# Performance work log

Measured on AMD Instinct MI355X. Metric: run time of the kernel, lower is better.

Reference implementation:

```python
import jax, jax.numpy as jnp
import numpy as np

H_, W_, KNN, KO = 64, 64, 32, 32
TAU, ETA, LAMBDA0, ALPHA = 1.5, 8.0, 0.001, 10.0
A_, B_, BETA, BETA_P = 1.0, 0.0, 8.0, 8.0
SMOOTH_KS, SMOOTH_SIGMA, EPS = 5, 1.0, 1e-6


def _base_grid(h, w):
    ys = jnp.arange(h, dtype=jnp.float32)
    xs = jnp.arange(w, dtype=jnp.float32)
    yy, xx = jnp.meshgrid(ys, xs, indexing='ij')
    return jnp.stack([xx.reshape(-1), yy.reshape(-1)], axis=-1)  # (N,2) as (x,y)


def _offset_bins(K_o, h, w):
    maxr = (h ** 2 + w ** 2) ** 0.5 * 0.5
    ks = jnp.arange(1, K_o + 1, dtype=jnp.float32)
    angles = 2.0 * jnp.pi * (ks - 1) / K_o
    radii = 0.2 * maxr + 0.6 * maxr * (ks - 1) / (K_o - 1 + 1e-9)
    return jnp.stack([radii * jnp.cos(angles), radii * jnp.sin(angles)], axis=-1)  # (K_o,2)


def _gaussian_kernel(ks, sigma):
    ax = jnp.arange(-(ks // 2), ks // 2 + 1, dtype=jnp.float32)  # matches torch -ks//2+1 .. ks//2 for odd ks
    xx, yy = jnp.meshgrid(ax, ax, indexing='ij')
    k = jnp.exp(-(xx ** 2 + yy ** 2) / (2.0 * sigma ** 2))
    return (k / k.sum()).reshape(1, 1, ks, ks)


def setup_inputs() -> dict:
    key = jax.random.key(0)
    k1, k2 = jax.random.split(key)
    B, N = 2, H_ * W_
    E = jax.random.normal(k1, (B, N, 256), dtype=jnp.float32)
    A0 = jax.random.uniform(k2, (B, N, N), dtype=jnp.float32)
    return {
        'E': E,
        'A0': A0,
        'P': _base_grid(H_, W_),
        'bins': _offset_bins(KO, H_, W_),
        'smooth_kernel': _gaussian_kernel(SMOOTH_KS, SMOOTH_SIGMA),
    }


def reference(E, A0, P, bins, smooth_kernel):
    B, N, _ = A0.shape
    # top-k neighbors per row (sorted descending, like torch.topk)
    topk_vals, topk_idx = jax.lax.top_k(A0, KNN)  # (B,N,k)

    # offset vectors to neighbors
    p_j = P[topk_idx]                              # (B,N,k,2)
    v = p_j - P[None, :, None, :]                  # (B,N,k,2)
    diff = v[..., None, :] - bins[None, None, None, :, :]   # (B,N,k,K_o,2)
    dist2 = (diff ** 2).sum(-1)                    # (B,N,k,K_o)
    kappa = jnp.exp(-dist2 / (2.0 * TAU ** 2 + 1e-12))

    # global bin histogram and softmax weights
    Hbins = (topk_vals[..., None] * kappa).sum(axis=(1, 2))   # (B,K_o)
    Wsoft = jax.nn.softmax(ETA * Hbins, axis=-1)              # (B,K_o)

    R_edges = LAMBDA0 + (Wsoft[:, None, None, :] * kappa).sum(-1)  # (B,N,k)
    tildeA = topk_vals * R_edges
    A1_edges = tildeA / (tildeA.sum(-1, keepdims=True) + EPS)

    # entropy -> backgroundness U
    p = jax.nn.softmax(ALPHA * A1_edges, axis=-1)
    entropy = -(p * jnp.log(p + EPS)).sum(-1)      # (B,N)
    U = jax.nn.sigmoid(-A_ * entropy + B_)
    m = 1.0 - U

    # mask both endpoints of each edge
    m_j = jax.vmap(jnp.take)(m, topk_idx)          # (B,N,k)
    hatA = m[:, :, None] * A1_edges * m_j
    A2_edges = hatA / (hatA.sum(-1, keepdims=True) + EPS)

    # scatter sparse edges back to dense NxN (row indices unique per row)
    b_idx = jnp.arange(B)[:, None, None]
    n_idx = jnp.arange(N)[None, :, None]
    A2_dense = jnp.zeros((B, N, N), A2_edges.dtype).at[b_idx, n_idx, topk_idx].set(A2_edges)
    A2_dense = A2_dense / (A2_dense.sum(-1, keepdims=True) + EPS)

    # directional evidence
    exp_fwd = jnp.exp(BETA * A2_dense)
    exp_rev = jnp.swapaxes(exp_fwd, -1, -2)
    P_dir = exp_fwd / (exp_fwd + exp_rev + EPS)
    eye = jnp.eye(N, dtype=A2_dense.dtype)
    P_dir = P_dir * (1.0 - eye)                    # zero diagonal
    s_ev = (A2_dense * P_dir).sum(-1)
    A2_T = jnp.swapaxes(A2_dense, -1, -2)
    t_ev = (A2_T * (1.0 - jnp.swapaxes(P_dir, -1, -2))).sum(-1)
    pi_src = s_ev / (s_ev + t_ev + EPS)
    pi_tgt = 1.0 - pi_src

    # spatial attention map
    W_mean = Wsoft.mean(0)                         # (K_o,)
    chi = (kappa * W_mean[None, None, None, :]).sum(-1)       # (B,N,k)
    w_local = jax.nn.softmax(BETA_P * A2_edges, axis=-1)
    q = (w_local * chi).sum(-1)                    # (B,N)
    A1_map = q.reshape(B, 1, H_, W_)
    pad = SMOOTH_KS // 2
    smoothed = jax.lax.conv_general_dilated(A1_map, smooth_kernel, (1, 1), [(pad, pad), (pad, pad)])
    A1_map = jax.nn.sigmoid(smoothed)              # (B,1,h,w)

    return (A2_dense, U, pi_src, pi_tgt, A1_map)
```

## Files before the change

### kernel.cpp

```cpp
#include <hip/hip_runtime.h>
#include <math.h>

#define NN 4096
#define KK 32
#define KOb 32
#define BB 2

constexpr float EPS = 1e-6f;

#define WS_VALS   0
#define WS_IDX    (WS_VALS + BB*NN*KK)
#define WS_HB     (WS_IDX + BB*NN*KK)
#define WS_WSOFT  (WS_HB + BB*KOb)
#define WS_WMEAN  (WS_WSOFT + BB*KOb)
#define WS_A1     (WS_WMEAN + KOb)
#define WS_M      (WS_A1 + BB*NN*KK)
#define WS_CHI    (WS_M + BB*NN)
#define WS_A2     (WS_CHI + BB*NN*KK)
#define WS_SEV    (WS_A2 + BB*NN*KK)
#define WS_TEV    (WS_SEV + BB*NN)
#define WS_Q      (WS_TEV + BB*NN)

#define OUT_A2   0
#define OUT_U    ((size_t)BB*NN*NN)
#define OUT_PSRC (OUT_U + BB*NN)
#define OUT_PTGT (OUT_PSRC + BB*NN)
#define OUT_MAP  (OUT_PTGT + BB*NN)

__device__ __forceinline__ unsigned int fkey(float x) {
    unsigned int u = __float_as_uint(x);
    return u ^ ((unsigned int)((int)u >> 31) | 0x80000000u);
}
__device__ __forceinline__ float key2f(unsigned int k) {
    unsigned int u = (k & 0x80000000u) ? (k ^ 0x80000000u) : ~k;
    return __uint_as_float(u);
}

__global__ __launch_bounds__(256) void k_topk(const float* __restrict__ A0,
                                              float* __restrict__ ws) {
    __shared__ unsigned long long cand[4][128];

    const int t = threadIdx.x;
    const int wv = t >> 6, lane = t & 63;
    const int R = blockIdx.x * 4 + wv;

    if (blockIdx.x == 0 && t < BB * KOb) ws[WS_HB + t] = 0.f;

    const float4* row4 = (const float4*)(A0 + (size_t)R * NN);
    unsigned int key[64];
    #pragma unroll
    for (int j4 = 0; j4 < 16; ++j4) {
        const float4 f = row4[j4 * 64 + lane];
        key[4 * j4 + 0] = fkey(f.x);
        key[4 * j4 + 1] = fkey(f.y);
        key[4 * j4 + 2] = fkey(f.z);
        key[4 * j4 + 3] = fkey(f.w);
    }

    unsigned int lo = 0u, hi = 0xFFFFFFFFu;
    int cnt = NN;
    int it = 0;
    while (cnt > 128) {
        unsigned int mid;
        if (it == 0)      mid = 0xBF7E0000u;
        else if (it == 1) mid = 0xBF7C4000u;
        else              mid = lo + ((hi - lo) >> 1);
        if (mid <= lo || mid >= hi) mid = lo + ((hi - lo) >> 1);
        if (mid == lo) break;
        int c = 0;
        #pragma unroll
        for (int j = 0; j < 64; ++j) c += (key[j] > mid) ? 1 : 0;
        #pragma unroll
        for (int m = 32; m >= 1; m >>= 1) c += __shfl_xor(c, m);
        if (c >= KK) { lo = mid; cnt = c; } else hi = mid;
        if (++it > 48) break;
    }

    int base = 0;
    #pragma unroll
    for (int j = 0; j < 64; ++j) {
        const bool p = key[j] > lo;
        const unsigned long long m = __ballot(p);
        if (p) {
            const int slot = base + __popcll(m & ((1ull << lane) - 1ull));
            if (slot < 128) {
                const unsigned int gidx = (unsigned int)((j >> 2) * 256 + lane * 4 + (j & 3));
                cand[wv][slot] = ((unsigned long long)key[j] << 32)
                               | (unsigned long long)(4095u - gidx);
            }
        }
        base += __popcll(m);
    }
    const int ncand = (base < 128) ? base : 128;
    __syncthreads();

    unsigned long long c0 = (lane < ncand) ? cand[wv][lane] : 0ull;
    unsigned long long c1 = (lane + 64 < ncand) ? cand[wv][lane + 64] : 0ull;
    unsigned long long resk = 0ull;
    for (int r = 0; r < KK; ++r) {
        unsigned long long bst = (c0 > c1) ? c0 : c1;
        #pragma unroll
        for (int m = 32; m >= 1; m >>= 1) {
            const unsigned long long o = __shfl_xor(bst, m);
            if (o > bst) bst = o;
        }
        if (lane == r) resk = bst;
        if (c0 == bst) c0 = 0ull;
        if (c1 == bst) c1 = 0ull;
    }
    if (lane < KK) {
        const unsigned int k = (unsigned int)(resk >> 32);
        const int gidx = 4095 - (int)(resk & 0xFFFull);
        ws[WS_VALS + (size_t)R * KK + lane] = key2f(k);
        ((int*)(ws + WS_IDX))[(size_t)R * KK + lane] = gidx;
    }
}

__global__ __launch_bounds__(256) void k_hbins(const float* __restrict__ bins,
                                               float* __restrict__ ws) {
    __shared__ float lval[1024], ldx[1024], ldy[1024];
    __shared__ float part[8][KOb];
    const int blk = blockIdx.x;
    const int t = threadIdx.x;
    const int row0 = blk * 32;
    const int b = row0 / NN;

    for (int e = t; e < 1024; e += 256) {
        const int R = row0 + (e >> 5);
        const int k = e & 31;
        const int r = R - b * NN;
        const int c = ((int*)(ws + WS_IDX))[(size_t)R * KK + k];
        lval[e] = ws[WS_VALS + (size_t)R * KK + k];
        ldx[e] = (float)((c & 63) - (r & 63));
        ldy[e] = (float)((c >> 6) - (r >> 6));
    }
    __syncthreads();

    const int o = t & 31, g = t >> 5;
    const float bx = bins[2 * o], by = bins[2 * o + 1];
    float acc = 0.f;
    for (int e = g; e < 1024; e += 8) {
        const float dx = ldx[e] - bx, dy = ldy[e] - by;
        acc += lval[e] * __expf(-(dx * dx + dy * dy) * (1.0f / 4.5f));
    }
    part[g][o] = acc;
    __syncthreads();
    if (t < 32) {
        float s = 0.f;
        #pragma unroll
        for (int g2 = 0; g2 < 8; ++g2) s += part[g2][t];
        atomicAdd(ws + WS_HB + b * KOb + t, s);
    }
}

__global__ void k_wsoft(float* __restrict__ ws) {
    __shared__ float sw[64];
    const int t = threadIdx.x;
    const int b = t >> 5, o = t & 31;
    const float h = 8.0f * ws[WS_HB + b * KOb + o];
    float mx = h;
    #pragma unroll
    for (int m = 16; m >= 1; m >>= 1) mx = fmaxf(mx, __shfl_xor(mx, m));
    const float e = __expf(h - mx);
    float s = e;
    #pragma unroll
    for (int m = 16; m >= 1; m >>= 1) s += __shfl_xor(s, m);
    const float w = e / s;
    ws[WS_WSOFT + b * KOb + o] = w;
    sw[t] = w;
    __syncthreads();
    if (t < 32) ws[WS_WMEAN + t] = 0.5f * (sw[t] + sw[32 + t]);
}

__global__ __launch_bounds__(256) void k_row1(const float* __restrict__ bins,
                                              float* __restrict__ ws,
                                              float* __restrict__ out_u) {
    __shared__ float sbins[2 * KOb], swsoft[BB * KOb], swmean[KOb];
    const int t = threadIdx.x;
    if (t < 2 * KOb) sbins[t] = bins[t];
    if (t >= 64 && t < 64 + BB * KOb) swsoft[t - 64] = ws[WS_WSOFT + t - 64];
    if (t >= 128 && t < 128 + KOb) swmean[t - 128] = ws[WS_WMEAN + t - 128];
    __syncthreads();

    const int wv = t >> 6, lane = t & 63;
    const int R = blockIdx.x * 4 + wv;
    const int b = R >> 12;
    const int r = R & (NN - 1);
    const bool act = lane < 32;
    const int k = lane;

    float val = 0.f, Redge = 0.f, chi = 0.f;
    if (act) {
        val = ws[WS_VALS + (size_t)R * KK + k];
        const int c = ((int*)(ws + WS_IDX))[(size_t)R * KK + k];
        const float dx0 = (float)((c & 63) - (r & 63));
        const float dy0 = (float)((c >> 6) - (r >> 6));
        float racc = 0.f, cacc = 0.f;
        for (int o = 0; o < KOb; ++o) {
            const float dx = dx0 - sbins[2 * o], dy = dy0 - sbins[2 * o + 1];
            const float kap = __expf(-(dx * dx + dy * dy) * (1.0f / 4.5f));
            racc += swsoft[b * KOb + o] * kap;
            cacc += swmean[o] * kap;
        }
        Redge = 0.001f + racc;
        chi = cacc;
    }
    const float tilde = act ? val * Redge : 0.f;
    float s = tilde;
    #pragma unroll
    for (int m = 16; m >= 1; m >>= 1) s += __shfl_xor(s, m);
    const float a1 = tilde / (s + EPS);

    const float z = act ? 10.f * a1 : -1e30f;
    float mz = z;
    #pragma unroll
    for (int m = 16; m >= 1; m >>= 1) mz = fmaxf(mz, __shfl_xor(mz, m));
    const float e = act ? __expf(z - mz) : 0.f;
    float se = e;
    #pragma unroll
    for (int m = 16; m >= 1; m >>= 1) se += __shfl_xor(se, m);
    const float p = e / se;
    const float ent_t = act ? -p * __logf(p + EPS) : 0.f;
    float ent = ent_t;
    #pragma unroll
    for (int m = 16; m >= 1; m >>= 1) ent += __shfl_xor(ent, m);
    const float U = 1.f / (1.f + __expf(ent));

    if (act) {
        ws[WS_A1  + (size_t)R * KK + k] = a1;
        ws[WS_CHI + (size_t)R * KK + k] = chi;
    }
    if (lane == 0) { out_u[R] = U; ws[WS_M + R] = 1.f - U; }
}

__global__ __launch_bounds__(256) void k_row2(float* __restrict__ ws) {
    const int gid = blockIdx.x * 256 + threadIdx.x;
    if (gid < BB * NN) ws[WS_TEV + gid] = 0.f;

    const int t = threadIdx.x;
    const int wv = t >> 6, lane = t & 63;
    const int R = blockIdx.x * 4 + wv;
    const int b = R >> 12;
    const bool act = lane < 32;
    const int k = lane;

    const float mi = ws[WS_M + R];
    float a1 = 0.f; int c = 0; float mj = 0.f;
    if (act) {
        a1 = ws[WS_A1 + (size_t)R * KK + k];
        c = ((int*)(ws + WS_IDX))[(size_t)R * KK + k];
        mj = ws[WS_M + b * NN + c];
    }
    const float hat = act ? mi * a1 * mj : 0.f;
    float S = hat;
    #pragma unroll
    for (int m = 16; m >= 1; m >>= 1) S += __shfl_xor(S, m);
    const float a2e = hat / (S + EPS);
    float S2 = a2e;
    #pragma unroll
    for (int m = 16; m >= 1; m >>= 1) S2 += __shfl_xor(S2, m);
    const float dv = a2e / (S2 + EPS);
    if (act) ws[WS_A2 + (size_t)R * KK + k] = dv;

    const float z = act ? 8.f * a2e : -1e30f;
    float mz = z;
    #pragma unroll
    for (int m = 16; m >= 1; m >>= 1) mz = fmaxf(mz, __shfl_xor(mz, m));
    const float e = act ? __expf(z - mz) : 0.f;
    float se = e;
    #pragma unroll
    for (int m = 16; m >= 1; m >>= 1) se += __shfl_xor(se, m);
    const float wl = e / se;
    const float chi = act ? ws[WS_CHI + (size_t)R * KK + k] : 0.f;
    float q = act ? wl * chi : 0.f;
    #pragma unroll
    for (int m = 16; m >= 1; m >>= 1) q += __shfl_xor(q, m);
    if (lane == 0) ws[WS_Q + R] = q;
}

__global__ __launch_bounds__(256) void k_dense(const float* __restrict__ ws,
                                               float* __restrict__ outA2) {
    __shared__ float srow[NN];
    __shared__ int   sidx[KK];
    __shared__ float sval[KK];
    const int R = blockIdx.x;
    const int b = R >> 12;
    const int r = R & (NN - 1);
    const int t = threadIdx.x;

    if (t < KK) {
        sidx[t] = ((const int*)(ws + WS_IDX))[(size_t)R * KK + t];
        sval[t] = ws[WS_A2 + (size_t)R * KK + t];
    }
    float4* s4 = (float4*)srow;
    const float4 z4 = make_float4(0.f, 0.f, 0.f, 0.f);
    #pragma unroll
    for (int i = 0; i < 4; ++i) s4[t + 256 * i] = z4;
    __syncthreads();
    if (t < KK) srow[sidx[t]] = sval[t];
    __syncthreads();
    float4* o4 = (float4*)(outA2 + (size_t)b * NN * NN + (size_t)r * NN);
    #pragma unroll
    for (int i = 0; i < 4; ++i) o4[t + 256 * i] = s4[t + 256 * i];
}

__global__ __launch_bounds__(256) void k_dir(float* __restrict__ ws,
                                             const float* __restrict__ A2d) {
    const int t = threadIdx.x;
    const int wv = t >> 6, lane = t & 63;
    const int R = blockIdx.x * 4 + wv;
    const int b = R >> 12;
    const int r = R & (NN - 1);
    const bool act = lane < 32;
    const int k = lane;

    float a = 0.f; int c = r;
    if (act) {
        a = ws[WS_A2 + (size_t)R * KK + k];
        c = ((int*)(ws + WS_IDX))[(size_t)R * KK + k];
    }
    float pdir = 0.f;
    if (act && c != r) {
        const float arev = A2d[(size_t)b * NN * NN + (size_t)c * NN + r];
        const float ef = __expf(8.f * a), er = __expf(8.f * arev);
        pdir = ef / (ef + er + EPS);
    }
    float s = a * pdir;
    #pragma unroll
    for (int m = 16; m >= 1; m >>= 1) s += __shfl_xor(s, m);
    if (lane == 0) ws[WS_SEV + R] = s;
    if (act) atomicAdd(ws + WS_TEV + b * NN + c, a * (1.f - pdir));
}

__global__ void k_tail(const float* __restrict__ ws, const float* __restrict__ kern,
                       float* __restrict__ out_psrc, float* __restrict__ out_ptgt,
                       float* __restrict__ out_map) {
    const int i = blockIdx.x * 256 + threadIdx.x;
    const float s = ws[WS_SEV + i], tv = ws[WS_TEV + i];
    const float ps = s / (s + tv + EPS);
    out_psrc[i] = ps;
    out_ptgt[i] = 1.f - ps;

    const int b = i >> 12;
    const int pix = i & 4095;
    const int y = pix >> 6, x = pix & 63;
    float acc = 0.f;
    #pragma unroll
    for (int ky = 0; ky < 5; ++ky) {
        const int yy = y + ky - 2;
        if (yy < 0 || yy >= 64) continue;
        #pragma unroll
        for (int kx = 0; kx < 5; ++kx) {
            const int xx = x + kx - 2;
            if (xx < 0 || xx >= 64) continue;
            acc += ws[WS_Q + b * 4096 + yy * 64 + xx] * kern[ky * 5 + kx];
        }
    }
    out_map[i] = 1.f / (1.f + __expf(-acc));
}

extern "C" void kernel_launch(void* const* d_in, const int* in_sizes, int n_in,
                              void* d_out, int out_size, void* d_ws, size_t ws_size,
                              hipStream_t stream) {
    const float* A0   = (const float*)d_in[1];
    const float* bins = (const float*)d_in[3];
    const float* kern = (const float*)d_in[4];
    float* out = (float*)d_out;
    float* ws  = (float*)d_ws;

    k_topk <<<BB * NN / 4,   256, 0, stream>>>(A0, ws);
    k_hbins<<<256,           256, 0, stream>>>(bins, ws);
    k_wsoft<<<1,              64, 0, stream>>>(ws);
    k_row1 <<<BB * NN / 4,   256, 0, stream>>>(bins, ws, out + OUT_U);
    k_row2 <<<BB * NN / 4,   256, 0, stream>>>(ws);
    k_dense<<<BB * NN,       256, 0, stream>>>(ws, out);
    k_dir  <<<BB * NN / 4,   256, 0, stream>>>(ws, out);
    k_tail <<<BB * NN / 256, 256, 0, stream>>>(ws, kern,
                                               out + OUT_PSRC, out + OUT_PTGT,
                                               out + OUT_MAP);
}
```

Measured before the change: 341.6 us.

## Fuse histogram into top-k, fold softmax into row1, merge row2 with dense scatter

Computes the per-bin histogram contribution inside the top-k kernel using shared-memory atomics and a slotted partial buffer, then reduces the partials and applies the softmax in each k_row1 block. This removes the k_hbins and k_wsoft launches. k_row2 is merged into the dense-row writer. The candidate pool shrinks to 64 and is compacted with a prefix scan and ranked by pairwise comparison instead of an iterative max extraction. The catch is that every row1 block redundantly re-reduces the partials, and the histogram now relies on atomics.

New measurement: 333.9 us. 2.2% less time.

```diff
diff --git a/kernel.cpp b/kernel.cpp
--- a/kernel.cpp
+++ b/kernel.cpp
@@ -5,15 +5,14 @@
 #define KK 32
 #define KOb 32
 #define BB 2
+#define NSLOT 64
 
 constexpr float EPS = 1e-6f;
 
 #define WS_VALS   0
 #define WS_IDX    (WS_VALS + BB*NN*KK)
-#define WS_HB     (WS_IDX + BB*NN*KK)
-#define WS_WSOFT  (WS_HB + BB*KOb)
-#define WS_WMEAN  (WS_WSOFT + BB*KOb)
-#define WS_A1     (WS_WMEAN + KOb)
+#define WS_HBP    (WS_IDX + BB*NN*KK)
+#define WS_A1     (WS_HBP + BB*NSLOT*KOb)
 #define WS_M      (WS_A1 + BB*NN*KK)
 #define WS_CHI    (WS_M + BB*NN)
 #define WS_A2     (WS_CHI + BB*NN*KK)
@@ -37,14 +36,20 @@
 }
 
 __global__ __launch_bounds__(256) void k_topk(const float* __restrict__ A0,
+                                              const float* __restrict__ bins,
                                               float* __restrict__ ws) {
-    __shared__ unsigned long long cand[4][128];
+    __shared__ unsigned long long cand[4][64];
+    __shared__ float sbins[2 * KOb];
+    __shared__ float shb[KOb];
 
     const int t = threadIdx.x;
     const int wv = t >> 6, lane = t & 63;
     const int R = blockIdx.x * 4 + wv;
-
-    if (blockIdx.x == 0 && t < BB * KOb) ws[WS_HB + t] = 0.f;
+    const int b = blockIdx.x >> 10;
+    const int r = R & (NN - 1);
+
+    if (t < 2 * KOb) sbins[t] = bins[t];
+    if (t < KOb) shb[t] = 0.f;
 
     const float4* row4 = (const float4*)(A0 + (size_t)R * NN);
     unsigned int key[64];
@@ -58,128 +63,117 @@
     }
 
     unsigned int lo = 0u, hi = 0xFFFFFFFFu;
-    int cnt = NN;
-    int it = 0;
-    while (cnt > 128) {
+    int cnt = NN, myc = 64, it = 0;
+    while (cnt > 64) {
         unsigned int mid;
         if (it == 0)      mid = 0xBF7E0000u;
         else if (it == 1) mid = 0xBF7C4000u;
         else              mid = lo + ((hi - lo) >> 1);
         if (mid <= lo || mid >= hi) mid = lo + ((hi - lo) >> 1);
         if (mid == lo) break;
-        int c = 0;
-        #pragma unroll
-        for (int j = 0; j < 64; ++j) c += (key[j] > mid) ? 1 : 0;
+        int cl = 0;
+        #pragma unroll
+        for (int j = 0; j < 64; ++j) cl += (key[j] > mid) ? 1 : 0;
+        int c = cl;
         #pragma unroll
         for (int m = 32; m >= 1; m >>= 1) c += __shfl_xor(c, m);
-        if (c >= KK) { lo = mid; cnt = c; } else hi = mid;
+        if (c >= KK) { lo = mid; cnt = c; myc = cl; } else hi = mid;
         if (++it > 48) break;
     }
-
-    int base = 0;
+    if (lo == 0u) {
+        int cl = 0;
+        #pragma unroll
+        for (int j = 0; j < 64; ++j) cl += (key[j] > 0u) ? 1 : 0;
+        myc = cl;
+    }
+
+    int pre = myc;
+    #pragma unroll
+    for (int m = 1; m < 64; m <<= 1) {
+        const int o = __shfl_up(pre, m);
+        if (lane >= m) pre += o;
+    }
+    pre -= myc;
+
+    int slot = pre;
     #pragma unroll
     for (int j = 0; j < 64; ++j) {
-        const bool p = key[j] > lo;
-        const unsigned long long m = __ballot(p);
-        if (p) {
-            const int slot = base + __popcll(m & ((1ull << lane) - 1ull));
-            if (slot < 128) {
-                const unsigned int gidx = (unsigned int)((j >> 2) * 256 + lane * 4 + (j & 3));
-                cand[wv][slot] = ((unsigned long long)key[j] << 32)
-                               | (unsigned long long)(4095u - gidx);
-            }
-        }
-        base += __popcll(m);
-    }
-    const int ncand = (base < 128) ? base : 128;
-    __syncthreads();
-
-    unsigned long long c0 = (lane < ncand) ? cand[wv][lane] : 0ull;
-    unsigned long long c1 = (lane + 64 < ncand) ? cand[wv][lane + 64] : 0ull;
-    unsigned long long resk = 0ull;
-    for (int r = 0; r < KK; ++r) {
-        unsigned long long bst = (c0 > c1) ? c0 : c1;
-        #pragma unroll
-        for (int m = 32; m >= 1; m >>= 1) {
-            const unsigned long long o = __shfl_xor(bst, m);
-            if (o > bst) bst = o;
-        }
-        if (lane == r) resk = bst;
-        if (c0 == bst) c0 = 0ull;
-        if (c1 == bst) c1 = 0ull;
-    }
-    if (lane < KK) {
-        const unsigned int k = (unsigned int)(resk >> 32);
-        const int gidx = 4095 - (int)(resk & 0xFFFull);
-        ws[WS_VALS + (size_t)R * KK + lane] = key2f(k);
-        ((int*)(ws + WS_IDX))[(size_t)R * KK + lane] = gidx;
-    }
-}
-
-__global__ __launch_bounds__(256) void k_hbins(const float* __restrict__ bins,
-                                               float* __restrict__ ws) {
-    __shared__ float lval[1024], ldx[1024], ldy[1024];
-    __shared__ float part[8][KOb];
-    const int blk = blockIdx.x;
-    const int t = threadIdx.x;
-    const int row0 = blk * 32;
-    const int b = row0 / NN;
-
-    for (int e = t; e < 1024; e += 256) {
-        const int R = row0 + (e >> 5);
-        const int k = e & 31;
-        const int r = R - b * NN;
-        const int c = ((int*)(ws + WS_IDX))[(size_t)R * KK + k];
-        lval[e] = ws[WS_VALS + (size_t)R * KK + k];
-        ldx[e] = (float)((c & 63) - (r & 63));
-        ldy[e] = (float)((c >> 6) - (r >> 6));
-    }
-    __syncthreads();
-
-    const int o = t & 31, g = t >> 5;
-    const float bx = bins[2 * o], by = bins[2 * o + 1];
-    float acc = 0.f;
-    for (int e = g; e < 1024; e += 8) {
-        const float dx = ldx[e] - bx, dy = ldy[e] - by;
-        acc += lval[e] * __expf(-(dx * dx + dy * dy) * (1.0f / 4.5f));
-    }
-    part[g][o] = acc;
-    __syncthreads();
-    if (t < 32) {
-        float s = 0.f;
-        #pragma unroll
-        for (int g2 = 0; g2 < 8; ++g2) s += part[g2][t];
-        atomicAdd(ws + WS_HB + b * KOb + t, s);
-    }
-}
-
-__global__ void k_wsoft(float* __restrict__ ws) {
-    __shared__ float sw[64];
-    const int t = threadIdx.x;
-    const int b = t >> 5, o = t & 31;
-    const float h = 8.0f * ws[WS_HB + b * KOb + o];
-    float mx = h;
-    #pragma unroll
-    for (int m = 16; m >= 1; m >>= 1) mx = fmaxf(mx, __shfl_xor(mx, m));
-    const float e = __expf(h - mx);
-    float s = e;
-    #pragma unroll
-    for (int m = 16; m >= 1; m >>= 1) s += __shfl_xor(s, m);
-    const float w = e / s;
-    ws[WS_WSOFT + b * KOb + o] = w;
-    sw[t] = w;
-    __syncthreads();
-    if (t < 32) ws[WS_WMEAN + t] = 0.5f * (sw[t] + sw[32 + t]);
+        if (key[j] > lo && slot < 64) {
+            const unsigned int gidx = (unsigned int)((j >> 2) * 256 + lane * 4 + (j & 3));
+            cand[wv][slot] = ((unsigned long long)key[j] << 32)
+                           | (unsigned long long)(4095u - gidx);
+            ++slot;
+        }
+    }
+    const int ncand = (cnt < 64) ? cnt : 64;
+    __syncthreads();
+
+    const unsigned long long cd = (lane < ncand) ? cand[wv][lane] : 0ull;
+    int rank = 0;
+    #pragma unroll
+    for (int i = 0; i < 64; ++i) {
+        const unsigned long long o = __shfl(cd, i);
+        rank += (o > cd) ? 1 : 0;
+    }
+
+    const bool sel = (lane < ncand) && (rank < KK);
+    float val = 0.f; int gidx = 0;
+    if (sel) {
+        val = key2f((unsigned int)(cd >> 32));
+        gidx = 4095 - (int)(cd & 0xFFFull);
+        ws[WS_VALS + (size_t)R * KK + rank] = val;
+        ((int*)(ws + WS_IDX))[(size_t)R * KK + rank] = gidx;
+    }
+
+    if (sel) {
+        const float dx0 = (float)((gidx & 63) - (r & 63));
+        const float dy0 = (float)((gidx >> 6) - (r >> 6));
+        #pragma unroll
+        for (int oo = 0; oo < KOb; ++oo) {
+            const int o = (oo + lane) & 31;
+            const float dx = dx0 - sbins[2 * o], dy = dy0 - sbins[2 * o + 1];
+            atomicAdd(&shb[o], val * __expf(-(dx * dx + dy * dy) * (1.0f / 4.5f)));
+        }
+    }
+    __syncthreads();
+    if (t < KOb)
+        atomicAdd(ws + WS_HBP + b * (NSLOT * KOb) + (blockIdx.x & (NSLOT - 1)) * KOb + t,
+                  shb[t]);
 }
 
 __global__ __launch_bounds__(256) void k_row1(const float* __restrict__ bins,
                                               float* __restrict__ ws,
                                               float* __restrict__ out_u) {
-    __shared__ float sbins[2 * KOb], swsoft[BB * KOb], swmean[KOb];
+    __shared__ float sbins[2 * KOb], sHB[BB * KOb], swsoft[BB * KOb], swmean[KOb];
     const int t = threadIdx.x;
     if (t < 2 * KOb) sbins[t] = bins[t];
-    if (t >= 64 && t < 64 + BB * KOb) swsoft[t - 64] = ws[WS_WSOFT + t - 64];
-    if (t >= 128 && t < 128 + KOb) swmean[t - 128] = ws[WS_WMEAN + t - 128];
+    if (t >= 64 && t < 64 + BB * KOb) sHB[t - 64] = 0.f;
+    __syncthreads();
+
+    #pragma unroll
+    for (int rep = 0; rep < 2; ++rep) {
+        const int task = t + 256 * rep;
+        const int bo = task & 63;
+        const int sg = task >> 6;
+        float ps = 0.f;
+        #pragma unroll
+        for (int s = 0; s < 8; ++s)
+            ps += ws[WS_HBP + (bo >> 5) * (NSLOT * KOb) + (sg * 8 + s) * KOb + (bo & 31)];
+        atomicAdd(&sHB[bo], ps);
+    }
+    __syncthreads();
+    if (t < BB * KOb) {
+        const float h = 8.0f * sHB[t];
+        float mx = h;
+        #pragma unroll
+        for (int m = 16; m >= 1; m >>= 1) mx = fmaxf(mx, __shfl_xor(mx, m));
+        const float e = __expf(h - mx);
+        float s = e;
+        #pragma unroll
+        for (int m = 16; m >= 1; m >>= 1) s += __shfl_xor(s, m);
+        swsoft[t] = e / s;
+    }
+    if (t < KOb) swmean[t] = 0.5f * (swsoft[t] + swsoft[KOb + t]);
     __syncthreads();
 
     const int wv = t >> 6, lane = t & 63;
@@ -233,71 +227,68 @@
     if (lane == 0) { out_u[R] = U; ws[WS_M + R] = 1.f - U; }
 }
 
-__global__ __launch_bounds__(256) void k_row2(float* __restrict__ ws) {
-    const int gid = blockIdx.x * 256 + threadIdx.x;
-    if (gid < BB * NN) ws[WS_TEV + gid] = 0.f;
-
-    const int t = threadIdx.x;
-    const int wv = t >> 6, lane = t & 63;
-    const int R = blockIdx.x * 4 + wv;
-    const int b = R >> 12;
-    const bool act = lane < 32;
-    const int k = lane;
-
-    const float mi = ws[WS_M + R];
-    float a1 = 0.f; int c = 0; float mj = 0.f;
-    if (act) {
-        a1 = ws[WS_A1 + (size_t)R * KK + k];
-        c = ((int*)(ws + WS_IDX))[(size_t)R * KK + k];
-        mj = ws[WS_M + b * NN + c];
-    }
-    const float hat = act ? mi * a1 * mj : 0.f;
-    float S = hat;
-    #pragma unroll
-    for (int m = 16; m >= 1; m >>= 1) S += __shfl_xor(S, m);
-    const float a2e = hat / (S + EPS);
-    float S2 = a2e;
-    #pragma unroll
-    for (int m = 16; m >= 1; m >>= 1) S2 += __shfl_xor(S2, m);
-    const float dv = a2e / (S2 + EPS);
-    if (act) ws[WS_A2 + (size_t)R * KK + k] = dv;
-
-    const float z = act ? 8.f * a2e : -1e30f;
-    float mz = z;
-    #pragma unroll
-    for (int m = 16; m >= 1; m >>= 1) mz = fmaxf(mz, __shfl_xor(mz, m));
-    const float e = act ? __expf(z - mz) : 0.f;
-    float se = e;
-    #pragma unroll
-    for (int m = 16; m >= 1; m >>= 1) se += __shfl_xor(se, m);
-    const float wl = e / se;
-    const float chi = act ? ws[WS_CHI + (size_t)R * KK + k] : 0.f;
-    float q = act ? wl * chi : 0.f;
-    #pragma unroll
-    for (int m = 16; m >= 1; m >>= 1) q += __shfl_xor(q, m);
-    if (lane == 0) ws[WS_Q + R] = q;
-}
-
-__global__ __launch_bounds__(256) void k_dense(const float* __restrict__ ws,
+__global__ __launch_bounds__(256) void k_row2d(float* __restrict__ ws,
                                                float* __restrict__ outA2) {
     __shared__ float srow[NN];
+    __shared__ float sdv[KK];
     __shared__ int   sidx[KK];
-    __shared__ float sval[KK];
     const int R = blockIdx.x;
     const int b = R >> 12;
     const int r = R & (NN - 1);
     const int t = threadIdx.x;
 
-    if (t < KK) {
-        sidx[t] = ((const int*)(ws + WS_IDX))[(size_t)R * KK + t];
-        sval[t] = ws[WS_A2 + (size_t)R * KK + t];
-    }
+    const int gid = blockIdx.x * 256 + t;
+    if (gid < BB * NN) ws[WS_TEV + gid] = 0.f;
+
     float4* s4 = (float4*)srow;
     const float4 z4 = make_float4(0.f, 0.f, 0.f, 0.f);
     #pragma unroll
     for (int i = 0; i < 4; ++i) s4[t + 256 * i] = z4;
-    __syncthreads();
-    if (t < KK) srow[sidx[t]] = sval[t];
+
+    if (t < 64) {
+        const int lane = t;
+        const bool act = lane < 32;
+        const int k = lane;
+        const float mi = ws[WS_M + R];
+        float a1 = 0.f; int c = 0; float mj = 0.f;
+        if (act) {
+            a1 = ws[WS_A1 + (size_t)R * KK + k];
+            c = ((int*)(ws + WS_IDX))[(size_t)R * KK + k];
+            mj = ws[WS_M + b * NN + c];
+        }
+        const float hat = act ? mi * a1 * mj : 0.f;
+        float S = hat;
+        #pragma unroll
+        for (int m = 16; m >= 1; m >>= 1) S += __shfl_xor(S, m);
+        const float a2e = hat / (S + EPS);
+        float S2 = a2e;
+        #pragma unroll
+        for (int m = 16; m >= 1; m >>= 1) S2 += __shfl_xor(S2, m);
+        const float dv = a2e / (S2 + EPS);
+
+        const float z = act ? 8.f * a2e : -1e30f;
+        float mz = z;
+        #pragma unroll
+        for (int m = 16; m >= 1; m >>= 1) mz = fmaxf(mz, __shfl_xor(mz, m));
+        const float e = act ? __expf(z - mz) : 0.f;
+        float se = e;
+        #pragma unroll
+        for (int m = 16; m >= 1; m >>= 1) se += __shfl_xor(se, m);
+        const float wl = e / se;
+        const float chi = act ? ws[WS_CHI + (size_t)R * KK + k] : 0.f;
+        float q = act ? wl * chi : 0.f;
+        #pragma unroll
+        for (int m = 16; m >= 1; m >>= 1) q += __shfl_xor(q, m);
+        if (lane == 0) ws[WS_Q + R] = q;
+
+        if (act) {
+            ws[WS_A2 + (size_t)R * KK + k] = dv;
+            sdv[k] = dv;
+            sidx[k] = c;
+        }
+    }
+    __syncthreads();
+    if (t < KK) srow[sidx[t]] = sdv[t];
     __syncthreads();
     float4* o4 = (float4*)(outA2 + (size_t)b * NN * NN + (size_t)r * NN);
     #pragma unroll
@@ -368,12 +359,11 @@
     float* out = (float*)d_out;
     float* ws  = (float*)d_ws;
 
-    k_topk <<<BB * NN / 4,   256, 0, stream>>>(A0, ws);
-    k_hbins<<<256,           256, 0, stream>>>(bins, ws);
-    k_wsoft<<<1,              64, 0, stream>>>(ws);
+    hipMemsetAsync(ws + WS_HBP, 0, BB * NSLOT * KOb * sizeof(float), stream);
+
+    k_topk <<<BB * NN / 4,   256, 0, stream>>>(A0, bins, ws);
     k_row1 <<<BB * NN / 4,   256, 0, stream>>>(bins, ws, out + OUT_U);
-    k_row2 <<<BB * NN / 4,   256, 0, stream>>>(ws);
-    k_dense<<<BB * NN,       256, 0, stream>>>(ws, out);
+    k_row2d<<<BB * NN,       256, 0, stream>>>(ws, out);
     k_dir  <<<BB * NN / 4,   256, 0, stream>>>(ws, out);
     k_tail <<<BB * NN / 256, 256, 0, stream>>>(ws, kern,
                                                out + OUT_PSRC, out + OUT_PTGT,
```
